# Kernel tuning notes

Measured on AMD Instinct MI355X. Metric: run time of the kernel, lower is better.

## Reference

```python
import jax, jax.numpy as jnp
import numpy as np

N_NODES = 100000

def setup_inputs() -> dict:
    key = jax.random.key(0)
    k1, k2, k3 = jax.random.split(key, 3)
    x = jax.random.normal(k1, (N_NODES, 64), dtype=jnp.float32)
    edge_index = jax.random.randint(k2, (2, 1250000), 0, N_NODES, dtype=jnp.int64)
    edge_weight = jax.random.uniform(k3, (1250000,), dtype=jnp.float32)
    return {"x": x, "edge_index": edge_index, "edge_weight": edge_weight}

def reference(x, edge_index, edge_weight):
    # LightGCNConv: out[dst] = sum_e edge_weight[e] * x[src_e]  (aggr='add')
    src, dst = edge_index[0], edge_index[1]
    msgs = edge_weight[:, None] * x[src]          # [E, d] gather-multiply
    out = jax.ops.segment_sum(msgs, dst, num_segments=N_NODES)  # scatter-add
    return out
```

## Files before the change

kernel.cpp:

```cpp
#include <hip/hip_runtime.h>
#include <hip/hip_bf16.h>


#define N_NODES   100000
#define N_FEAT    64

#define A_BSH     7
#define A_NPB     (1 << A_BSH)
#define A_KB      ((N_NODES + A_NPB - 1) >> A_BSH)
#define A_CAP     2048
#define A_FCHUNK  4096
#define A_OVCAP   65536
#define NBIN      ((1250000 + A_FCHUNK - 1) / A_FCHUNK)
#define NCAST     391

__global__ __launch_bounds__(1024) void k_castbin(
    const float* __restrict__ x, ushort* __restrict__ xb,
    const int* __restrict__ ei, const float* __restrict__ w,
    int* __restrict__ bcur, int2* __restrict__ stg,
    int* __restrict__ ovf, int* __restrict__ ovcnt, int E) {
    int t = threadIdx.x;
    if (blockIdx.x >= NBIN) {
        int cb = blockIdx.x - NBIN;
        #pragma unroll
        for (int k = 0; k < 4; ++k) {
            int i4 = cb * 4096 + k * 1024 + t;
            if (i4 < N_NODES * N_FEAT / 4) {
                float4 v = ((const float4*)x)[i4];
                uint4 u = *(uint4*)&v;
                ushort4 r;
                r.x = (ushort)((u.x + 0x7FFFu + ((u.x >> 16) & 1)) >> 16);
                r.y = (ushort)((u.y + 0x7FFFu + ((u.y >> 16) & 1)) >> 16);
                r.z = (ushort)((u.z + 0x7FFFu + ((u.z >> 16) & 1)) >> 16);
                r.w = (ushort)((u.w + 0x7FFFu + ((u.w >> 16) & 1)) >> 16);
                ((ushort4*)xb)[i4] = r;
            }
        }
        return;
    }
    __shared__ int h[A_KB];
    for (int b = t; b < A_KB; b += 1024) h[b] = 0;
    __syncthreads();
    int e0 = blockIdx.x * A_FCHUNK;
    int dstv[A_FCHUNK / 1024];
    int srcv[A_FCHUNK / 1024];
    float wv[A_FCHUNK / 1024];
    #pragma unroll
    for (int k = 0; k < A_FCHUNK / 1024; ++k) {
        int e = e0 + k * 1024 + t;
        bool ok = (e < E);
        dstv[k] = ok ? ei[E + e] : -1;
        srcv[k] = ok ? ei[e] : 0;
        wv[k]   = ok ? w[e] : 0.f;
        if (ok) atomicAdd(&h[dstv[k] >> A_BSH], 1);
    }
    __syncthreads();
    for (int b = t; b < A_KB; b += 1024) {
        int c = h[b];
        h[b] = c ? atomicAdd(&bcur[b], c) : 0;
    }
    __syncthreads();
    #pragma unroll
    for (int k = 0; k < A_FCHUNK / 1024; ++k) {
        if (dstv[k] >= 0) {
            int b = dstv[k] >> A_BSH;
            int loc = atomicAdd(&h[b], 1);
            if (loc < A_CAP) {
                stg[b * A_CAP + loc] =
                    make_int2(srcv[k] | ((dstv[k] & (A_NPB - 1)) << 17),
                              __float_as_int(wv[k]));
            } else {
                int oi = atomicAdd(ovcnt, 1);
                if (oi < A_OVCAP) ovf[oi] = e0 + k * 1024 + t;
            }
        }
    }
}

__global__ __launch_bounds__(512, 8) void k_sortgather(
    const ushort* __restrict__ xb, const int* __restrict__ bcur,
    const int2* __restrict__ stg, float* __restrict__ out,
    const float* __restrict__ x, const int* __restrict__ ei,
    const float* __restrict__ w, const int* __restrict__ ovf,
    const int* __restrict__ ovcnt, int E) {
    __shared__ int2 buf[A_CAP];
    __shared__ int2 srt[A_CAP];
    __shared__ int  hist[A_NPB];
    __shared__ int  start[A_NPB];
    __shared__ int  cur[A_NPB];
    __shared__ int  ovn;
    int b = blockIdx.x, t = threadIdx.x;
    int cnt = bcur[b];
    if (cnt > A_CAP) cnt = A_CAP;
    int base = b * A_CAP;

    if (t < A_NPB) hist[t] = 0;
    if (t == 0) { int n = *ovcnt; ovn = (n > A_OVCAP) ? A_OVCAP : n; }
    __syncthreads();
    for (int i = t; i < cnt; i += 512) {
        int2 p = stg[base + i];
        buf[i] = p;
        atomicAdd(&hist[(p.x >> 17) & (A_NPB - 1)], 1);
    }
    __syncthreads();
    if (t < 64) {
        int s0 = hist[2 * t], s1 = hist[2 * t + 1];
        int ps = s0 + s1;
        #pragma unroll
        for (int off = 1; off < 64; off <<= 1) {
            int v = __shfl_up(ps, off);
            if (t >= off) ps += v;
        }
        int excl = ps - (s0 + s1);
        start[2 * t]     = excl;       cur[2 * t]     = excl;
        start[2 * t + 1] = excl + s0;  cur[2 * t + 1] = excl + s0;
    }
    __syncthreads();
    for (int i = t; i < cnt; i += 512) {
        int2 p = buf[i];
        int pos = atomicAdd(&cur[(p.x >> 17) & (A_NPB - 1)], 1);
        srt[pos] = p;
    }
    __syncthreads();

    int wid  = t >> 6;
    int lane = t & 63;
    int q    = lane >> 4;
    int l    = lane & 15;
    const ushort4* xb4 = (const ushort4*)xb;
    int novf = ovn;
    #pragma unroll
    for (int pass = 0; pass < 4; ++pass) {
        int n = pass * 32 + wid * 4 + q;
        int node = (b << A_BSH) + n;
        int j = start[n], end = start[n] + hist[n];
        float ax0 = 0.f, ay0 = 0.f, az0 = 0.f, aw0 = 0.f;
        float ax1 = 0.f, ay1 = 0.f, az1 = 0.f, aw1 = 0.f;
        for (; j + 1 < end; j += 2) {
            int2 p0 = srt[j];
            int2 p1 = srt[j + 1];
            ushort4 u0 = xb4[(size_t)(p0.x & 0x1FFFF) * 16 + l];
            ushort4 u1 = xb4[(size_t)(p1.x & 0x1FFFF) * 16 + l];
            float w0 = __int_as_float(p0.y), w1 = __int_as_float(p1.y);
            ax0 += w0 * __uint_as_float((uint)u0.x << 16);
            ay0 += w0 * __uint_as_float((uint)u0.y << 16);
            az0 += w0 * __uint_as_float((uint)u0.z << 16);
            aw0 += w0 * __uint_as_float((uint)u0.w << 16);
            ax1 += w1 * __uint_as_float((uint)u1.x << 16);
            ay1 += w1 * __uint_as_float((uint)u1.y << 16);
            az1 += w1 * __uint_as_float((uint)u1.z << 16);
            aw1 += w1 * __uint_as_float((uint)u1.w << 16);
        }
        if (j < end) {
            int2 p = srt[j];
            ushort4 u = xb4[(size_t)(p.x & 0x1FFFF) * 16 + l];
            float wv = __int_as_float(p.y);
            ax0 += wv * __uint_as_float((uint)u.x << 16);
            ay0 += wv * __uint_as_float((uint)u.y << 16);
            az0 += wv * __uint_as_float((uint)u.z << 16);
            aw0 += wv * __uint_as_float((uint)u.w << 16);
        }
        if (novf) {
            for (int i = 0; i < novf; ++i) {
                int e = ovf[i];
                if (ei[E + e] == node) {
                    float wv = w[e];
                    float4 xv = ((const float4*)x)[(size_t)ei[e] * 16 + l];
                    ax0 += wv * xv.x; ay0 += wv * xv.y;
                    az0 += wv * xv.z; aw0 += wv * xv.w;
                }
            }
        }
        if (node < N_NODES) {
            float4 r;
            r.x = ax0 + ax1; r.y = ay0 + ay1;
            r.z = az0 + az1; r.w = aw0 + aw1;
            ((float4*)out)[(size_t)node * 16 + l] = r;
        }
    }
}

#define BSH       8
#define NPB       (1 << BSH)
#define KB        ((N_NODES + NPB - 1) >> BSH)
#define FCHUNK    8192
#define SORT_CAP  4096

__global__ __launch_bounds__(256) void k_chist(
    const int* __restrict__ ei, int* __restrict__ bcur, int E) {
    __shared__ int h[KB];
    int t = threadIdx.x;
    for (int b = t; b < KB; b += 256) h[b] = 0;
    __syncthreads();
    int e0 = blockIdx.x * FCHUNK;
    #pragma unroll
    for (int k = 0; k < FCHUNK / 256; ++k) {
        int e = e0 + k * 256 + t;
        if (e < E) atomicAdd(&h[ei[E + e] >> BSH], 1);
    }
    __syncthreads();
    for (int b = t; b < KB; b += 256) if (h[b]) atomicAdd(&bcur[b], h[b]);
}

__global__ __launch_bounds__(256) void k_cscan(
    int* __restrict__ bcur, int* __restrict__ boffs) {
    __shared__ int sdata[256];
    int t = threadIdx.x;
    int i0 = 2 * t, i1 = 2 * t + 1;
    int v0 = (i0 < KB) ? bcur[i0] : 0;
    int v1 = (i1 < KB) ? bcur[i1] : 0;
    sdata[t] = v0 + v1; __syncthreads();
    for (int off = 1; off < 256; off <<= 1) {
        int v = (t >= off) ? sdata[t - off] : 0;
        __syncthreads();
        if (t >= off) sdata[t] += v;
        __syncthreads();
    }
    int run = (t == 0) ? 0 : sdata[t - 1];
    if (i0 < KB) { boffs[i0] = run; bcur[i0] = run; }
    run += v0;
    if (i1 < KB) { boffs[i1] = run; bcur[i1] = run; }
    if (t == 255) boffs[KB] = sdata[255];
}

__global__ __launch_bounds__(256) void k_cbin(
    const int* __restrict__ ei, const float* __restrict__ w,
    int* __restrict__ bcur, int2* __restrict__ stg, int E) {
    __shared__ int h[KB];
    int t = threadIdx.x;
    for (int b = t; b < KB; b += 256) h[b] = 0;
    __syncthreads();
    int e0 = blockIdx.x * FCHUNK;
    #pragma unroll
    for (int k = 0; k < FCHUNK / 256; ++k) {
        int e = e0 + k * 256 + t;
        if (e < E) atomicAdd(&h[ei[E + e] >> BSH], 1);
    }
    __syncthreads();
    for (int b = t; b < KB; b += 256) {
        int c = h[b];
        h[b] = c ? atomicAdd(&bcur[b], c) : 0;
    }
    __syncthreads();
    #pragma unroll
    for (int k = 0; k < FCHUNK / 256; ++k) {
        int e = e0 + k * 256 + t;
        if (e < E) {
            int dst = ei[E + e];
            int slot = atomicAdd(&h[dst >> BSH], 1);
            stg[slot] = make_int2(ei[e] | ((dst & (NPB - 1)) << 17),
                                  __float_as_int(w[e]));
        }
    }
}

__global__ __launch_bounds__(256) void k_csort(
    int2* __restrict__ stg, const int* __restrict__ boffs,
    int* __restrict__ offs) {
    __shared__ int2 buf[SORT_CAP];
    __shared__ int  hist[NPB];
    __shared__ int  cur[NPB];
    __shared__ int  sdata[256];
    int b = blockIdx.x, t = threadIdx.x;
    int bg = boffs[b], end = boffs[b + 1], cnt = end - bg;
    for (int n = t; n < NPB; n += 256) hist[n] = 0;
    __syncthreads();
    int nlds = cnt < SORT_CAP ? cnt : SORT_CAP;
    for (int i = t; i < nlds; i += 256) {
        int2 p = stg[bg + i];
        buf[i] = p;
        atomicAdd(&hist[(p.x >> 17) & (NPB - 1)], 1);
    }
    int2 r0{0,0}, r1{0,0}; int nr = 0;
    {
        int i0 = nlds + t, i1 = nlds + 256 + t;
        if (i0 < cnt) { r0 = stg[bg + i0]; atomicAdd(&hist[(r0.x >> 17) & (NPB - 1)], 1); nr = 1; }
        if (i1 < cnt) { r1 = stg[bg + i1]; atomicAdd(&hist[(r1.x >> 17) & (NPB - 1)], 1); nr = 2; }
    }
    __syncthreads();
    int c = hist[t];
    sdata[t] = c; __syncthreads();
    for (int off = 1; off < 256; off <<= 1) {
        int v = (t >= off) ? sdata[t - off] : 0;
        __syncthreads();
        if (t >= off) sdata[t] += v;
        __syncthreads();
    }
    int excl = (t == 0) ? 0 : sdata[t - 1];
    cur[t] = excl;
    int node = (b << BSH) + t;
    if (node < N_NODES) offs[node] = bg + excl;
    if (b == KB - 1 && t == 255) offs[N_NODES] = end;
    __syncthreads();
    for (int i = t; i < nlds; i += 256) {
        int2 p = buf[i];
        int pos = atomicAdd(&cur[(p.x >> 17) & (NPB - 1)], 1);
        stg[bg + pos] = p;
    }
    if (nr >= 1) { int pos = atomicAdd(&cur[(r0.x >> 17) & (NPB - 1)], 1); stg[bg + pos] = r0; }
    if (nr >= 2) { int pos = atomicAdd(&cur[(r1.x >> 17) & (NPB - 1)], 1); stg[bg + pos] = r1; }
}

__global__ __launch_bounds__(256) void k_gather(
    const float* __restrict__ x, const int* __restrict__ offs,
    const int2* __restrict__ stg, float* __restrict__ out) {
    int node = blockIdx.x * 4 + (threadIdx.x >> 6);
    int lane = threadIdx.x & 63;
    if (node >= N_NODES) return;
    int bg = offs[node], end = offs[node + 1];
    float a0 = 0.f, a1 = 0.f, a2 = 0.f, a3 = 0.f;
    int j = bg;
    for (; j + 3 < end; j += 4) {
        int2 p0 = stg[j];
        int2 p1 = stg[j + 1];
        int2 p2 = stg[j + 2];
        int2 p3 = stg[j + 3];
        a0 += __int_as_float(p0.y) * x[(size_t)(p0.x & 0x1FFFF) * N_FEAT + lane];
        a1 += __int_as_float(p1.y) * x[(size_t)(p1.x & 0x1FFFF) * N_FEAT + lane];
        a2 += __int_as_float(p2.y) * x[(size_t)(p2.x & 0x1FFFF) * N_FEAT + lane];
        a3 += __int_as_float(p3.y) * x[(size_t)(p3.x & 0x1FFFF) * N_FEAT + lane];
    }
    for (; j < end; ++j) {
        int2 p = stg[j];
        a0 += __int_as_float(p.y) * x[(size_t)(p.x & 0x1FFFF) * N_FEAT + lane];
    }
    out[(size_t)node * N_FEAT + lane] = (a0 + a1) + (a2 + a3);
}

__global__ __launch_bounds__(256) void gnn_scatter_kernel(
    const float* __restrict__ x, const int* __restrict__ ei,
    const float* __restrict__ w, float* __restrict__ out, int E) {
    int e = blockIdx.x * 4 + (threadIdx.x >> 6);
    int lane = threadIdx.x & 63;
    if (e >= E) return;
    float v = w[e] * x[(size_t)ei[e] * N_FEAT + lane];
    atomicAdd(&out[(size_t)ei[E + e] * N_FEAT + lane], v);
}

static inline size_t align16(size_t v) { return (v + 15) & ~(size_t)15; }

extern "C" void kernel_launch(void* const* d_in, const int* in_sizes, int n_in,
                              void* d_out, int out_size, void* d_ws, size_t ws_size,
                              hipStream_t stream) {
    const float* x   = (const float*)d_in[0];
    const int*   ei  = (const int*)d_in[1];
    const float* w   = (const float*)d_in[2];
    float*       out = (float*)d_out;
    const int E = in_sizes[2];
    char* ws = (char*)d_ws;

    size_t a_xb   = 0;
    size_t a_stg  = align16(a_xb + (size_t)N_NODES * N_FEAT * 2);
    size_t a_bcur = align16(a_stg + (size_t)A_KB * A_CAP * 8);
    size_t a_ovf  = align16(a_bcur + (size_t)(A_KB + 1) * 4);
    size_t need_a = a_ovf + (size_t)A_OVCAP * 4;

    if (ws_size >= need_a && E == 1250000) {
        ushort* xb    = (ushort*)(ws + a_xb);
        int2*   stg   = (int2*)(ws + a_stg);
        int*    bcur  = (int*)(ws + a_bcur);
        int*    ovcnt = bcur + A_KB;
        int*    ovf   = (int*)(ws + a_ovf);

        hipMemsetAsync(bcur, 0, (size_t)(A_KB + 1) * 4, stream);
        k_castbin<<<NBIN + NCAST, 1024, 0, stream>>>(
            x, xb, ei, w, bcur, stg, ovf, ovcnt, E);
        k_sortgather<<<A_KB, 512, 0, stream>>>(
            xb, bcur, stg, out, x, ei, w, ovf, ovcnt, E);
        return;
    }

    size_t b_bcur  = 0;
    size_t b_boffs = align16(b_bcur + (size_t)KB * 4);
    size_t b_offs  = align16(b_boffs + (size_t)(KB + 1) * 4);
    size_t b_stg   = align16(b_offs + (size_t)(N_NODES + 1) * 4);
    size_t need_b  = b_stg + (size_t)E * 8;

    if (ws_size >= need_b) {
        int*  bcur  = (int*)(ws + b_bcur);
        int*  boffs = (int*)(ws + b_boffs);
        int*  offs  = (int*)(ws + b_offs);
        int2* stg   = (int2*)(ws + b_stg);
        const int nblk = (E + FCHUNK - 1) / FCHUNK;
        hipMemsetAsync(bcur, 0, (size_t)KB * 4, stream);
        k_chist<<<nblk, 256, 0, stream>>>(ei, bcur, E);
        k_cscan<<<1, 256, 0, stream>>>(bcur, boffs);
        k_cbin<<<nblk, 256, 0, stream>>>(ei, w, bcur, stg, E);
        k_csort<<<KB, 256, 0, stream>>>(stg, boffs, offs);
        k_gather<<<(N_NODES + 3) / 4, 256, 0, stream>>>(x, offs, stg, out);
        return;
    }

    hipMemsetAsync(d_out, 0, (size_t)out_size * sizeof(float), stream);
    gnn_scatter_kernel<<<(E + 3) / 4, 256, 0, stream>>>(x, ei, w, out, E);
}
```

Measured before the change: 131.4 us.

## Replace bucket binning and in-block sort with per-node fixed-capacity edge slots

Each edge now takes a global atomic slot directly in its destination node's fixed 64-entry staging row. This replaces per-block histograms, 128-node buckets and the shared-memory counting sort in the gather kernel. The gather kernel assigns one wavefront per node, splits that node's edges across four 16-lane groups, and combines the partial sums with shuffles. The intent is to drop the sort phase and its shared-memory traffic. In exchange it issues 1.25M contended global atomics, makes scattered 8-byte writes into a much larger staging buffer, and leaves many slots unused.

Result: slower. 207.4 us (+57.9%).

```diff
diff --git a/kernel.cpp b/kernel.cpp
--- a/kernel.cpp
+++ b/kernel.cpp
@@ -5,10 +5,7 @@
 #define N_NODES   100000
 #define N_FEAT    64
 
-#define A_BSH     7
-#define A_NPB     (1 << A_BSH)
-#define A_KB      ((N_NODES + A_NPB - 1) >> A_BSH)
-#define A_CAP     2048
+#define A_DCAP    64
 #define A_FCHUNK  4096
 #define A_OVCAP   65536
 #define NBIN      ((1250000 + A_FCHUNK - 1) / A_FCHUNK)
@@ -17,7 +14,7 @@
 __global__ __launch_bounds__(1024) void k_castbin(
     const float* __restrict__ x, ushort* __restrict__ xb,
     const int* __restrict__ ei, const float* __restrict__ w,
-    int* __restrict__ bcur, int2* __restrict__ stg,
+    int* __restrict__ dcnt, int2* __restrict__ stg,
     int* __restrict__ ovf, int* __restrict__ ovcnt, int E) {
     int t = threadIdx.x;
     if (blockIdx.x >= NBIN) {
@@ -38,145 +35,71 @@
         }
         return;
     }
-    __shared__ int h[A_KB];
-    for (int b = t; b < A_KB; b += 1024) h[b] = 0;
-    __syncthreads();
     int e0 = blockIdx.x * A_FCHUNK;
-    int dstv[A_FCHUNK / 1024];
-    int srcv[A_FCHUNK / 1024];
-    float wv[A_FCHUNK / 1024];
     #pragma unroll
     for (int k = 0; k < A_FCHUNK / 1024; ++k) {
         int e = e0 + k * 1024 + t;
-        bool ok = (e < E);
-        dstv[k] = ok ? ei[E + e] : -1;
-        srcv[k] = ok ? ei[e] : 0;
-        wv[k]   = ok ? w[e] : 0.f;
-        if (ok) atomicAdd(&h[dstv[k] >> A_BSH], 1);
-    }
-    __syncthreads();
-    for (int b = t; b < A_KB; b += 1024) {
-        int c = h[b];
-        h[b] = c ? atomicAdd(&bcur[b], c) : 0;
-    }
-    __syncthreads();
-    #pragma unroll
-    for (int k = 0; k < A_FCHUNK / 1024; ++k) {
-        if (dstv[k] >= 0) {
-            int b = dstv[k] >> A_BSH;
-            int loc = atomicAdd(&h[b], 1);
-            if (loc < A_CAP) {
-                stg[b * A_CAP + loc] =
-                    make_int2(srcv[k] | ((dstv[k] & (A_NPB - 1)) << 17),
-                              __float_as_int(wv[k]));
+        if (e < E) {
+            int dst = ei[E + e];
+            int src = ei[e];
+            float wv = w[e];
+            int slot = atomicAdd(&dcnt[dst], 1);
+            if (slot < A_DCAP) {
+                stg[(size_t)dst * A_DCAP + slot] =
+                    make_int2(src, __float_as_int(wv));
             } else {
                 int oi = atomicAdd(ovcnt, 1);
-                if (oi < A_OVCAP) ovf[oi] = e0 + k * 1024 + t;
+                if (oi < A_OVCAP) ovf[oi] = e;
             }
         }
     }
 }
 
-__global__ __launch_bounds__(512, 8) void k_sortgather(
-    const ushort* __restrict__ xb, const int* __restrict__ bcur,
+__global__ __launch_bounds__(256) void k_ngather(
+    const ushort* __restrict__ xb, const int* __restrict__ dcnt,
     const int2* __restrict__ stg, float* __restrict__ out,
     const float* __restrict__ x, const int* __restrict__ ei,
     const float* __restrict__ w, const int* __restrict__ ovf,
     const int* __restrict__ ovcnt, int E) {
-    __shared__ int2 buf[A_CAP];
-    __shared__ int2 srt[A_CAP];
-    __shared__ int  hist[A_NPB];
-    __shared__ int  start[A_NPB];
-    __shared__ int  cur[A_NPB];
-    __shared__ int  ovn;
-    int b = blockIdx.x, t = threadIdx.x;
-    int cnt = bcur[b];
-    if (cnt > A_CAP) cnt = A_CAP;
-    int base = b * A_CAP;
-
-    if (t < A_NPB) hist[t] = 0;
-    if (t == 0) { int n = *ovcnt; ovn = (n > A_OVCAP) ? A_OVCAP : n; }
-    __syncthreads();
-    for (int i = t; i < cnt; i += 512) {
-        int2 p = stg[base + i];
-        buf[i] = p;
-        atomicAdd(&hist[(p.x >> 17) & (A_NPB - 1)], 1);
-    }
-    __syncthreads();
-    if (t < 64) {
-        int s0 = hist[2 * t], s1 = hist[2 * t + 1];
-        int ps = s0 + s1;
-        #pragma unroll
-        for (int off = 1; off < 64; off <<= 1) {
-            int v = __shfl_up(ps, off);
-            if (t >= off) ps += v;
-        }
-        int excl = ps - (s0 + s1);
-        start[2 * t]     = excl;       cur[2 * t]     = excl;
-        start[2 * t + 1] = excl + s0;  cur[2 * t + 1] = excl + s0;
-    }
-    __syncthreads();
-    for (int i = t; i < cnt; i += 512) {
-        int2 p = buf[i];
-        int pos = atomicAdd(&cur[(p.x >> 17) & (A_NPB - 1)], 1);
-        srt[pos] = p;
-    }
-    __syncthreads();
-
-    int wid  = t >> 6;
-    int lane = t & 63;
+    int node = blockIdx.x * 4 + (threadIdx.x >> 6);
+    if (node >= N_NODES) return;
+    int lane = threadIdx.x & 63;
     int q    = lane >> 4;
     int l    = lane & 15;
+    int cnt = dcnt[node];
+    int c = cnt < A_DCAP ? cnt : A_DCAP;
+    const int2*    ps  = &stg[(size_t)node * A_DCAP];
     const ushort4* xb4 = (const ushort4*)xb;
-    int novf = ovn;
-    #pragma unroll
-    for (int pass = 0; pass < 4; ++pass) {
-        int n = pass * 32 + wid * 4 + q;
-        int node = (b << A_BSH) + n;
-        int j = start[n], end = start[n] + hist[n];
-        float ax0 = 0.f, ay0 = 0.f, az0 = 0.f, aw0 = 0.f;
-        float ax1 = 0.f, ay1 = 0.f, az1 = 0.f, aw1 = 0.f;
-        for (; j + 1 < end; j += 2) {
-            int2 p0 = srt[j];
-            int2 p1 = srt[j + 1];
-            ushort4 u0 = xb4[(size_t)(p0.x & 0x1FFFF) * 16 + l];
-            ushort4 u1 = xb4[(size_t)(p1.x & 0x1FFFF) * 16 + l];
-            float w0 = __int_as_float(p0.y), w1 = __int_as_float(p1.y);
-            ax0 += w0 * __uint_as_float((uint)u0.x << 16);
-            ay0 += w0 * __uint_as_float((uint)u0.y << 16);
-            az0 += w0 * __uint_as_float((uint)u0.z << 16);
-            aw0 += w0 * __uint_as_float((uint)u0.w << 16);
-            ax1 += w1 * __uint_as_float((uint)u1.x << 16);
-            ay1 += w1 * __uint_as_float((uint)u1.y << 16);
-            az1 += w1 * __uint_as_float((uint)u1.z << 16);
-            aw1 += w1 * __uint_as_float((uint)u1.w << 16);
-        }
-        if (j < end) {
-            int2 p = srt[j];
-            ushort4 u = xb4[(size_t)(p.x & 0x1FFFF) * 16 + l];
-            float wv = __int_as_float(p.y);
-            ax0 += wv * __uint_as_float((uint)u.x << 16);
-            ay0 += wv * __uint_as_float((uint)u.y << 16);
-            az0 += wv * __uint_as_float((uint)u.z << 16);
-            aw0 += wv * __uint_as_float((uint)u.w << 16);
-        }
-        if (novf) {
-            for (int i = 0; i < novf; ++i) {
+    float ax = 0.f, ay = 0.f, az = 0.f, aw = 0.f;
+    for (int j = q; j < c; j += 4) {
+        int2 p = ps[j];
+        ushort4 u = xb4[(size_t)p.x * 16 + l];
+        float wv = __int_as_float(p.y);
+        ax += wv * __uint_as_float((uint)u.x << 16);
+        ay += wv * __uint_as_float((uint)u.y << 16);
+        az += wv * __uint_as_float((uint)u.z << 16);
+        aw += wv * __uint_as_float((uint)u.w << 16);
+    }
+    ax += __shfl_xor(ax, 16); ax += __shfl_xor(ax, 32);
+    ay += __shfl_xor(ay, 16); ay += __shfl_xor(ay, 32);
+    az += __shfl_xor(az, 16); az += __shfl_xor(az, 32);
+    aw += __shfl_xor(aw, 16); aw += __shfl_xor(aw, 32);
+    if (lane < 16) {
+        float4 r; r.x = ax; r.y = ay; r.z = az; r.w = aw;
+        int ovn = *ovcnt;
+        if (ovn) {
+            if (ovn > A_OVCAP) ovn = A_OVCAP;
+            for (int i = 0; i < ovn; ++i) {
                 int e = ovf[i];
                 if (ei[E + e] == node) {
                     float wv = w[e];
                     float4 xv = ((const float4*)x)[(size_t)ei[e] * 16 + l];
-                    ax0 += wv * xv.x; ay0 += wv * xv.y;
-                    az0 += wv * xv.z; aw0 += wv * xv.w;
+                    r.x += wv * xv.x; r.y += wv * xv.y;
+                    r.z += wv * xv.z; r.w += wv * xv.w;
                 }
             }
         }
-        if (node < N_NODES) {
-            float4 r;
-            r.x = ax0 + ax1; r.y = ay0 + ay1;
-            r.z = az0 + az1; r.w = aw0 + aw1;
-            ((float4*)out)[(size_t)node * 16 + l] = r;
-        }
+        ((float4*)out)[(size_t)node * 16 + l] = r;
     }
 }
 
@@ -351,22 +274,22 @@
 
     size_t a_xb   = 0;
     size_t a_stg  = align16(a_xb + (size_t)N_NODES * N_FEAT * 2);
-    size_t a_bcur = align16(a_stg + (size_t)A_KB * A_CAP * 8);
-    size_t a_ovf  = align16(a_bcur + (size_t)(A_KB + 1) * 4);
+    size_t a_dcnt = align16(a_stg + (size_t)N_NODES * A_DCAP * 8);
+    size_t a_ovf  = align16(a_dcnt + (size_t)(N_NODES + 1) * 4);
     size_t need_a = a_ovf + (size_t)A_OVCAP * 4;
 
     if (ws_size >= need_a && E == 1250000) {
         ushort* xb    = (ushort*)(ws + a_xb);
         int2*   stg   = (int2*)(ws + a_stg);
-        int*    bcur  = (int*)(ws + a_bcur);
-        int*    ovcnt = bcur + A_KB;
+        int*    dcnt  = (int*)(ws + a_dcnt);
+        int*    ovcnt = dcnt + N_NODES;
         int*    ovf   = (int*)(ws + a_ovf);
 
-        hipMemsetAsync(bcur, 0, (size_t)(A_KB + 1) * 4, stream);
+        hipMemsetAsync(dcnt, 0, (size_t)(N_NODES + 1) * 4, stream);
         k_castbin<<<NBIN + NCAST, 1024, 0, stream>>>(
-            x, xb, ei, w, bcur, stg, ovf, ovcnt, E);
-        k_sortgather<<<A_KB, 512, 0, stream>>>(
-            xb, bcur, stg, out, x, ei, w, ovf, ovcnt, E);
+            x, xb, ei, w, dcnt, stg, ovf, ovcnt, E);
+        k_ngather<<<(N_NODES + 3) / 4, 256, 0, stream>>>(
+            xb, dcnt, stg, out, x, ei, w, ovf, ovcnt, E);
         return;
     }
 
```
